# Kernel optimization log

Hardware: AMD Instinct MI355X
Metric: run time of the kernel (lower is better)

## Reference

```python
import jax, jax.numpy as jnp
import numpy as np

LORA_ALPHA = 16.0
TOP_K = 2


def setup_inputs() -> dict:
    key = jax.random.key(0)
    k_x, k_w, k_g, k_a, k_b = jax.random.split(key, 5)
    B, S, H, O, E, R = 2, 2048, 2048, 2048, 8, 16
    x = jax.random.normal(k_x, (B, S, H), dtype=jnp.float32)
    weight = jax.random.normal(k_w, (O, H), dtype=jnp.float32)          # frozen base W [out, in]
    gate_w = jax.random.normal(k_g, (E, H), dtype=jnp.float32) * 0.02   # router gate [E, in]
    A_w = jax.random.normal(k_a, (E, R, H), dtype=jnp.float32) * (1.0 / np.sqrt(H))  # stacked lora_A
    B_w = jax.random.normal(k_b, (E, O, R), dtype=jnp.float32) * 0.01   # stacked lora_B
    return {"x": x, "weight": weight, "gate_w": gate_w, "A_w": A_w, "B_w": B_w}


def reference(x, weight, gate_w, A_w, B_w):
    E = gate_w.shape[0]
    # Base frozen linear: F.linear(x, weight)
    out = jnp.einsum("bsh,oh->bso", x, weight)

    # Router: softmax over experts, top-2, renormalize
    logits = jnp.einsum("bsh,eh->bse", x, gate_w)
    probs = jax.nn.softmax(logits, axis=-1)
    topk_w, topk_idx = jax.lax.top_k(probs, TOP_K)          # [b,s,2]
    topk_w = topk_w / jnp.sum(topk_w, axis=-1, keepdims=True)

    # Per-token combine weight for each expert (sum over the 2 slots)
    onehot = jax.nn.one_hot(topk_idx, E, dtype=x.dtype)      # [b,s,2,E]
    cw = jnp.einsum("bsk,bske->bse", topk_w, onehot)         # [b,s,E]

    # LoRA: down-project into all experts' rank spaces, weight, then up-project.
    # t: [b,s,E,r] is small (r=16); weighting here avoids a [b,s,E,out] buffer.
    t = jnp.einsum("bsh,erh->bser", x, A_w)
    t = t * cw[..., None]
    lora = jnp.einsum("bser,eor->bso", t, B_w)

    return out + LORA_ALPHA * lora
```

## Files before the change

kernel.cpp:

```cpp
#include <hip/hip_runtime.h>
#include <hip/hip_bf16.h>


typedef __bf16 bf16x8 __attribute__((ext_vector_type(8)));
typedef float f32x4 __attribute__((ext_vector_type(4)));

__device__ __forceinline__ __bf16 f2bf(float f) {
  union { float f; unsigned u; } v; v.f = f;
  unsigned r = (v.u + 0x7FFFu + ((v.u >> 16) & 1u)) >> 16;
  unsigned short s = (unsigned short)r;
  return __builtin_bit_cast(__bf16, s);
}

__device__ __forceinline__ void ld_lds16(const void* g, void* l) {
  __builtin_amdgcn_global_load_lds((__attribute__((address_space(1))) void*)g,
                                   (__attribute__((address_space(3))) void*)l,
                                   16, 0, 0);
}

__global__ void prep_kernel(const float* __restrict__ W, const float* __restrict__ Aw,
                            const float* __restrict__ Bw, __bf16* __restrict__ Bfull,
                            __bf16* __restrict__ A2) {
  const int b = blockIdx.x, tid = threadIdx.x;
  if (b < 2176) {
    const float* src = (b < 2048) ? (W + (size_t)b * 2048)
                                  : (Aw + (size_t)(b - 2048) * 2048);
    __bf16* dst = (b < 2048) ? (Bfull + (size_t)b * 2176)
                             : (A2 + (size_t)(b - 2048) * 2048);
    const int c = tid * 8;
    float4 a = *(const float4*)(src + c);
    float4 d = *(const float4*)(src + c + 4);
    bf16x8 v;
    v[0] = f2bf(a.x); v[1] = f2bf(a.y); v[2] = f2bf(a.z); v[3] = f2bf(a.w);
    v[4] = f2bf(d.x); v[5] = f2bf(d.y); v[6] = f2bf(d.z); v[7] = f2bf(d.w);
    *(bf16x8*)(dst + c) = v;
  } else {
    const int idx = (b - 2176) * 256 + tid;
    const int e = idx >> 11, o = idx & 2047;
    const float4* s = (const float4*)(Bw + ((size_t)e * 2048 + o) * 16);
    float4 v0 = s[0], v1 = s[1], v2 = s[2], v3 = s[3];
    __bf16* d = Bfull + (size_t)o * 2176 + 2048 + e * 16;
    bf16x8 lo, hi;
    lo[0] = f2bf(v0.x); lo[1] = f2bf(v0.y); lo[2] = f2bf(v0.z); lo[3] = f2bf(v0.w);
    lo[4] = f2bf(v1.x); lo[5] = f2bf(v1.y); lo[6] = f2bf(v1.z); lo[7] = f2bf(v1.w);
    hi[0] = f2bf(v2.x); hi[1] = f2bf(v2.y); hi[2] = f2bf(v2.z); hi[3] = f2bf(v2.w);
    hi[4] = f2bf(v3.x); hi[5] = f2bf(v3.y); hi[6] = f2bf(v3.z); hi[7] = f2bf(v3.w);
    *(bf16x8*)d = lo;
    *(bf16x8*)(d + 8) = hi;
  }
}

__global__ __launch_bounds__(256) void router_t2(
    const float* __restrict__ x, const float* __restrict__ gw,
    const __bf16* __restrict__ A2, __bf16* __restrict__ Abuf) {
  __shared__ __align__(16) __bf16 xs[16][2056];
  __shared__ float red[4][16][8];
  __shared__ float cws[16][8];
  const int tid = threadIdx.x;
  const int wave = tid >> 6, lane = tid & 63;
  const int t0 = blockIdx.x * 16;

#pragma unroll 4
  for (int i = 0; i < 16; ++i) {
    const float* xr = x + (size_t)(t0 + i) * 2048 + tid * 8;
    float4 a = *(const float4*)xr;
    float4 b = *(const float4*)(xr + 4);
    bf16x8 v;
    v[0] = f2bf(a.x); v[1] = f2bf(a.y); v[2] = f2bf(a.z); v[3] = f2bf(a.w);
    v[4] = f2bf(b.x); v[5] = f2bf(b.y); v[6] = f2bf(b.z); v[7] = f2bf(b.w);
    *(bf16x8*)(Abuf + (size_t)(t0 + i) * 2176 + tid * 8) = v;
    *(bf16x8*)&xs[i][tid * 8] = v;
  }
  __syncthreads();

  const int tok = tid & 15, slc = tid >> 4;
  const int c0 = slc * 128;
  float acc[8] = {0, 0, 0, 0, 0, 0, 0, 0};
  for (int j8 = 0; j8 < 16; ++j8) {
    bf16x8 xv = *(const bf16x8*)&xs[tok][c0 + j8 * 8];
    float xf[8];
#pragma unroll
    for (int j = 0; j < 8; ++j) xf[j] = (float)xv[j];
#pragma unroll
    for (int e = 0; e < 8; ++e) {
      float4 g0 = *(const float4*)(gw + e * 2048 + c0 + j8 * 8);
      float4 g1 = *(const float4*)(gw + e * 2048 + c0 + j8 * 8 + 4);
      acc[e] += xf[0] * g0.x + xf[1] * g0.y + xf[2] * g0.z + xf[3] * g0.w +
                xf[4] * g1.x + xf[5] * g1.y + xf[6] * g1.z + xf[7] * g1.w;
    }
  }
#pragma unroll
  for (int e = 0; e < 8; ++e) {
    acc[e] += __shfl_down(acc[e], 16);
    acc[e] += __shfl_down(acc[e], 32);
  }
  if (lane < 16) {
#pragma unroll
    for (int e = 0; e < 8; ++e) red[wave][lane][e] = acc[e];
  }
  __syncthreads();
  if (tid < 16) {
    float lg[8];
#pragma unroll
    for (int e = 0; e < 8; ++e)
      lg[e] = red[0][tid][e] + red[1][tid][e] + red[2][tid][e] + red[3][tid][e];
    int a = 0;
    for (int e = 1; e < 8; ++e) if (lg[e] > lg[a]) a = e;
    int b = (a == 0) ? 1 : 0;
    for (int e = 0; e < 8; ++e) if (e != a && lg[e] > lg[b]) b = e;
    const float d = __expf(lg[b] - lg[a]);
    float o[8] = {0, 0, 0, 0, 0, 0, 0, 0};
    o[a] = 1.0f / (1.0f + d);
    o[b] = d / (1.0f + d);
#pragma unroll
    for (int e = 0; e < 8; ++e) cws[tid][e] = o[e];
  }
  __syncthreads();

  const int m = lane & 15, q = lane >> 4;
  const int nt0 = wave * 2;
  f32x4 tacc[2] = {};
  for (int ks = 0; ks < 64; ++ks) {
    bf16x8 af = *(const bf16x8*)&xs[m][ks * 32 + q * 8];
#pragma unroll
    for (int h = 0; h < 2; ++h) {
      bf16x8 bfg = *(const bf16x8*)(A2 + (size_t)((nt0 + h) * 16 + m) * 2048 +
                                    ks * 32 + q * 8);
      tacc[h] = __builtin_amdgcn_mfma_f32_16x16x32_bf16(af, bfg, tacc[h], 0, 0, 0);
    }
  }
#pragma unroll
  for (int h = 0; h < 2; ++h) {
    const int nt = nt0 + h;
#pragma unroll
    for (int rg = 0; rg < 4; ++rg) {
      const int trow = q * 4 + rg;
      const float s = tacc[h][rg] * 16.0f * cws[trow][nt];
      Abuf[(size_t)(t0 + trow) * 2176 + 2048 + nt * 16 + m] = f2bf(s);
    }
  }
}

__global__ __launch_bounds__(128, 2) void mfma_gemm_bt(
    const __bf16* __restrict__ A, const __bf16* __restrict__ B,
    float* __restrict__ C, int lda, int ldb, int ldc, int kiters) {
  __shared__ __align__(16) __bf16 As[128 * 64];
  __shared__ __align__(16) __bf16 Bs[64 * 64];
  const int tid = threadIdx.x;
  const int wave = tid >> 6;
  const int lane = tid & 63;
  const int tm = blockIdx.x * 128;
  const int tn = blockIdx.y * 64;

  const int wm = wave * 64;
  const int srow = lane >> 3;
  const int skoff = ((lane & 7) ^ srow) * 8;

  const int rlo = lane & 7;
  const int rb3 = (lane >> 3) & 1;
  const int qb = lane >> 4;

  f32x4 acc[4][4] = {};

  int kcur = 0;
  for (int kt = 0; kt < kiters; ++kt) {
#pragma unroll
    for (int r = 0; r < 8; ++r) {
      const int ch = r * 2 + wave;
      ld_lds16(A + (size_t)(tm + ch * 8 + srow) * lda + kcur + skoff, &As[ch * 512]);
    }
#pragma unroll
    for (int r = 0; r < 4; ++r) {
      const int ch = r * 2 + wave;
      ld_lds16(B + (size_t)(tn + ch * 8 + srow) * ldb + kcur + skoff, &Bs[ch * 512]);
    }
    __syncthreads();
#pragma unroll
    for (int ks = 0; ks < 2; ++ks) {
      bf16x8 af[4], bfg[4];
      const int q8 = ((ks * 4 + qb) ^ rlo) * 8;
#pragma unroll
      for (int i = 0; i < 4; ++i) {
        const int rh = ((wm + i * 16) >> 3) + rb3;
        af[i] = *(const bf16x8*)&As[rh * 512 + rlo * 64 + q8];
      }
#pragma unroll
      for (int j = 0; j < 4; ++j) {
        const int rh = ((j * 16) >> 3) + rb3;
        bfg[j] = *(const bf16x8*)&Bs[rh * 512 + rlo * 64 + q8];
      }
#pragma unroll
      for (int i = 0; i < 4; ++i)
#pragma unroll
        for (int j = 0; j < 4; ++j)
          acc[i][j] = __builtin_amdgcn_mfma_f32_16x16x32_bf16(af[i], bfg[j], acc[i][j], 0, 0, 0);
    }
    __syncthreads();
    kcur += 64;
  }

  const int crow0 = tm + wm + (lane >> 4) * 4;
  const int ccol0 = tn + (lane & 15);
#pragma unroll
  for (int i = 0; i < 4; ++i)
#pragma unroll
    for (int j = 0; j < 4; ++j)
#pragma unroll
      for (int rg = 0; rg < 4; ++rg)
        C[(size_t)(crow0 + i * 16 + rg) * ldc + ccol0 + j * 16] = acc[i][j][rg];
}

extern "C" void kernel_launch(void* const* d_in, const int* in_sizes, int n_in,
                              void* d_out, int out_size, void* d_ws, size_t ws_size,
                              hipStream_t stream) {
  const float* x = (const float*)d_in[0];
  const float* weight = (const float*)d_in[1];
  const float* gate_w = (const float*)d_in[2];
  const float* A_w = (const float*)d_in[3];
  const float* B_w = (const float*)d_in[4];
  float* out = (float*)d_out;

  char* ws = (char*)d_ws;
  __bf16* Abuf = (__bf16*)ws;
  __bf16* Bfull = (__bf16*)(ws + 17825792);
  __bf16* A2 = (__bf16*)(ws + 26738688);

  prep_kernel<<<2240, 256, 0, stream>>>(weight, A_w, B_w, Bfull, A2);
  router_t2<<<256, 256, 0, stream>>>(x, gate_w, A2, Abuf);
  mfma_gemm_bt<<<dim3(32, 32), 128, 0, stream>>>(Abuf, Bfull, out, 2176, 2176,
                                                 2048, 34);
}
```

Before: 166.5 us.

## Split router into convert/route and LoRA-down kernels; use four waves in GEMM

```diff
diff --git a/kernel.cpp b/kernel.cpp
--- a/kernel.cpp
+++ b/kernel.cpp
@@ -50,60 +50,62 @@
   }
 }
 
-__global__ __launch_bounds__(256) void router_t2(
+__global__ __launch_bounds__(256) void conv_router(
     const float* __restrict__ x, const float* __restrict__ gw,
-    const __bf16* __restrict__ A2, __bf16* __restrict__ Abuf) {
-  __shared__ __align__(16) __bf16 xs[16][2056];
-  __shared__ float red[4][16][8];
-  __shared__ float cws[16][8];
+    __bf16* __restrict__ Abuf, float* __restrict__ cw) {
+  __shared__ float red[256][17];
+  __shared__ float red2[16][17];
   const int tid = threadIdx.x;
-  const int wave = tid >> 6, lane = tid & 63;
-  const int t0 = blockIdx.x * 16;
-
-#pragma unroll 4
-  for (int i = 0; i < 16; ++i) {
-    const float* xr = x + (size_t)(t0 + i) * 2048 + tid * 8;
-    float4 a = *(const float4*)xr;
-    float4 b = *(const float4*)(xr + 4);
-    bf16x8 v;
-    v[0] = f2bf(a.x); v[1] = f2bf(a.y); v[2] = f2bf(a.z); v[3] = f2bf(a.w);
-    v[4] = f2bf(b.x); v[5] = f2bf(b.y); v[6] = f2bf(b.z); v[7] = f2bf(b.w);
-    *(bf16x8*)(Abuf + (size_t)(t0 + i) * 2176 + tid * 8) = v;
-    *(bf16x8*)&xs[i][tid * 8] = v;
-  }
+  const int t0 = blockIdx.x * 2;
+  const int c = tid * 8;
+
+  float4 a0 = *(const float4*)(x + (size_t)t0 * 2048 + c);
+  float4 b0 = *(const float4*)(x + (size_t)t0 * 2048 + c + 4);
+  float4 a1 = *(const float4*)(x + (size_t)(t0 + 1) * 2048 + c);
+  float4 b1 = *(const float4*)(x + (size_t)(t0 + 1) * 2048 + c + 4);
+  float xf0[8] = {a0.x, a0.y, a0.z, a0.w, b0.x, b0.y, b0.z, b0.w};
+  float xf1[8] = {a1.x, a1.y, a1.z, a1.w, b1.x, b1.y, b1.z, b1.w};
+
+  bf16x8 v0, v1;
+#pragma unroll
+  for (int j = 0; j < 8; ++j) { v0[j] = f2bf(xf0[j]); v1[j] = f2bf(xf1[j]); }
+  *(bf16x8*)(Abuf + (size_t)t0 * 2176 + c) = v0;
+  *(bf16x8*)(Abuf + (size_t)(t0 + 1) * 2176 + c) = v1;
+
+  float acc0[8], acc1[8];
+#pragma unroll
+  for (int e = 0; e < 8; ++e) { acc0[e] = 0.0f; acc1[e] = 0.0f; }
+#pragma unroll
+  for (int e = 0; e < 8; ++e) {
+    float4 g0 = *(const float4*)(gw + e * 2048 + c);
+    float4 g1 = *(const float4*)(gw + e * 2048 + c + 4);
+    float gg[8] = {g0.x, g0.y, g0.z, g0.w, g1.x, g1.y, g1.z, g1.w};
+#pragma unroll
+    for (int j = 0; j < 8; ++j) {
+      acc0[e] += xf0[j] * gg[j];
+      acc1[e] += xf1[j] * gg[j];
+    }
+  }
+#pragma unroll
+  for (int e = 0; e < 8; ++e) { red[tid][e] = acc0[e]; red[tid][8 + e] = acc1[e]; }
   __syncthreads();
-
-  const int tok = tid & 15, slc = tid >> 4;
-  const int c0 = slc * 128;
-  float acc[8] = {0, 0, 0, 0, 0, 0, 0, 0};
-  for (int j8 = 0; j8 < 16; ++j8) {
-    bf16x8 xv = *(const bf16x8*)&xs[tok][c0 + j8 * 8];
-    float xf[8];
-#pragma unroll
-    for (int j = 0; j < 8; ++j) xf[j] = (float)xv[j];
+  {
+    const int p = tid & 15, ch = tid >> 4;
+    float s = 0.0f;
+#pragma unroll
+    for (int i = 0; i < 16; ++i) s += red[ch * 16 + i][p];
+    red2[ch][p] = s;
+  }
+  __syncthreads();
+  if (tid < 2) {
+    float lg[8];
 #pragma unroll
     for (int e = 0; e < 8; ++e) {
-      float4 g0 = *(const float4*)(gw + e * 2048 + c0 + j8 * 8);
-      float4 g1 = *(const float4*)(gw + e * 2048 + c0 + j8 * 8 + 4);
-      acc[e] += xf[0] * g0.x + xf[1] * g0.y + xf[2] * g0.z + xf[3] * g0.w +
-                xf[4] * g1.x + xf[5] * g1.y + xf[6] * g1.z + xf[7] * g1.w;
-    }
-  }
-#pragma unroll
-  for (int e = 0; e < 8; ++e) {
-    acc[e] += __shfl_down(acc[e], 16);
-    acc[e] += __shfl_down(acc[e], 32);
-  }
-  if (lane < 16) {
-#pragma unroll
-    for (int e = 0; e < 8; ++e) red[wave][lane][e] = acc[e];
-  }
-  __syncthreads();
-  if (tid < 16) {
-    float lg[8];
-#pragma unroll
-    for (int e = 0; e < 8; ++e)
-      lg[e] = red[0][tid][e] + red[1][tid][e] + red[2][tid][e] + red[3][tid][e];
+      float s = 0.0f;
+#pragma unroll
+      for (int ch = 0; ch < 16; ++ch) s += red2[ch][tid * 8 + e];
+      lg[e] = s;
+    }
     int a = 0;
     for (int e = 1; e < 8; ++e) if (lg[e] > lg[a]) a = e;
     int b = (a == 0) ? 1 : 0;
@@ -112,36 +114,41 @@
     float o[8] = {0, 0, 0, 0, 0, 0, 0, 0};
     o[a] = 1.0f / (1.0f + d);
     o[b] = d / (1.0f + d);
-#pragma unroll
-    for (int e = 0; e < 8; ++e) cws[tid][e] = o[e];
-  }
-  __syncthreads();
-
+    const int t = t0 + tid;
+#pragma unroll
+    for (int e = 0; e < 8; ++e) cw[t * 8 + e] = o[e];
+  }
+}
+
+__global__ __launch_bounds__(256) void t2_scale(
+    const __bf16* __restrict__ Abuf_x, const __bf16* __restrict__ A2,
+    const float* __restrict__ cw, __bf16* __restrict__ Abuf) {
+  const int tid = threadIdx.x;
+  const int wave = tid >> 6, lane = tid & 63;
+  const int t0 = blockIdx.x * 16;
+  const int jg = blockIdx.y * 4 + wave;
   const int m = lane & 15, q = lane >> 4;
-  const int nt0 = wave * 2;
-  f32x4 tacc[2] = {};
-  for (int ks = 0; ks < 64; ++ks) {
-    bf16x8 af = *(const bf16x8*)&xs[m][ks * 32 + q * 8];
-#pragma unroll
-    for (int h = 0; h < 2; ++h) {
-      bf16x8 bfg = *(const bf16x8*)(A2 + (size_t)((nt0 + h) * 16 + m) * 2048 +
-                                    ks * 32 + q * 8);
-      tacc[h] = __builtin_amdgcn_mfma_f32_16x16x32_bf16(af, bfg, tacc[h], 0, 0, 0);
-    }
-  }
-#pragma unroll
-  for (int h = 0; h < 2; ++h) {
-    const int nt = nt0 + h;
-#pragma unroll
-    for (int rg = 0; rg < 4; ++rg) {
-      const int trow = q * 4 + rg;
-      const float s = tacc[h][rg] * 16.0f * cws[trow][nt];
-      Abuf[(size_t)(t0 + trow) * 2176 + 2048 + nt * 16 + m] = f2bf(s);
-    }
-  }
-}
-
-__global__ __launch_bounds__(128, 2) void mfma_gemm_bt(
+
+  const __bf16* arow = Abuf_x + (size_t)(t0 + m) * 2176 + q * 8;
+  const __bf16* brow = A2 + (size_t)(jg * 16 + m) * 2048 + q * 8;
+  f32x4 acc0 = {}, acc1 = {};
+  for (int ks = 0; ks < 64; ks += 2) {
+    bf16x8 af0 = *(const bf16x8*)(arow + ks * 32);
+    bf16x8 bf0 = *(const bf16x8*)(brow + ks * 32);
+    bf16x8 af1 = *(const bf16x8*)(arow + ks * 32 + 32);
+    bf16x8 bf1 = *(const bf16x8*)(brow + ks * 32 + 32);
+    acc0 = __builtin_amdgcn_mfma_f32_16x16x32_bf16(af0, bf0, acc0, 0, 0, 0);
+    acc1 = __builtin_amdgcn_mfma_f32_16x16x32_bf16(af1, bf1, acc1, 0, 0, 0);
+  }
+#pragma unroll
+  for (int rg = 0; rg < 4; ++rg) {
+    const int t = t0 + q * 4 + rg;
+    const float s = (acc0[rg] + acc1[rg]) * 16.0f * cw[t * 8 + jg];
+    Abuf[(size_t)t * 2176 + 2048 + jg * 16 + m] = f2bf(s);
+  }
+}
+
+__global__ __launch_bounds__(256, 4) void mfma_gemm_bt(
     const __bf16* __restrict__ A, const __bf16* __restrict__ B,
     float* __restrict__ C, int lda, int ldb, int ldc, int kiters) {
   __shared__ __align__(16) __bf16 As[128 * 64];
@@ -152,7 +159,8 @@
   const int tm = blockIdx.x * 128;
   const int tn = blockIdx.y * 64;
 
-  const int wm = wave * 64;
+  const int wm = (wave >> 1) * 64;
+  const int wn = (wave & 1) * 32;
   const int srow = lane >> 3;
   const int skoff = ((lane & 7) ^ srow) * 8;
 
@@ -160,24 +168,24 @@
   const int rb3 = (lane >> 3) & 1;
   const int qb = lane >> 4;
 
-  f32x4 acc[4][4] = {};
+  f32x4 acc[4][2] = {};
 
   int kcur = 0;
   for (int kt = 0; kt < kiters; ++kt) {
 #pragma unroll
-    for (int r = 0; r < 8; ++r) {
-      const int ch = r * 2 + wave;
+    for (int r = 0; r < 4; ++r) {
+      const int ch = r * 4 + wave;
       ld_lds16(A + (size_t)(tm + ch * 8 + srow) * lda + kcur + skoff, &As[ch * 512]);
     }
 #pragma unroll
-    for (int r = 0; r < 4; ++r) {
-      const int ch = r * 2 + wave;
+    for (int r = 0; r < 2; ++r) {
+      const int ch = r * 4 + wave;
       ld_lds16(B + (size_t)(tn + ch * 8 + srow) * ldb + kcur + skoff, &Bs[ch * 512]);
     }
     __syncthreads();
 #pragma unroll
     for (int ks = 0; ks < 2; ++ks) {
-      bf16x8 af[4], bfg[4];
+      bf16x8 af[4], bfg[2];
       const int q8 = ((ks * 4 + qb) ^ rlo) * 8;
 #pragma unroll
       for (int i = 0; i < 4; ++i) {
@@ -185,14 +193,14 @@
         af[i] = *(const bf16x8*)&As[rh * 512 + rlo * 64 + q8];
       }
 #pragma unroll
-      for (int j = 0; j < 4; ++j) {
-        const int rh = ((j * 16) >> 3) + rb3;
+      for (int j = 0; j < 2; ++j) {
+        const int rh = ((wn + j * 16) >> 3) + rb3;
         bfg[j] = *(const bf16x8*)&Bs[rh * 512 + rlo * 64 + q8];
       }
 #pragma unroll
       for (int i = 0; i < 4; ++i)
 #pragma unroll
-        for (int j = 0; j < 4; ++j)
+        for (int j = 0; j < 2; ++j)
           acc[i][j] = __builtin_amdgcn_mfma_f32_16x16x32_bf16(af[i], bfg[j], acc[i][j], 0, 0, 0);
     }
     __syncthreads();
@@ -200,11 +208,11 @@
   }
 
   const int crow0 = tm + wm + (lane >> 4) * 4;
-  const int ccol0 = tn + (lane & 15);
+  const int ccol0 = tn + wn + (lane & 15);
 #pragma unroll
   for (int i = 0; i < 4; ++i)
 #pragma unroll
-    for (int j = 0; j < 4; ++j)
+    for (int j = 0; j < 2; ++j)
 #pragma unroll
       for (int rg = 0; rg < 4; ++rg)
         C[(size_t)(crow0 + i * 16 + rg) * ldc + ccol0 + j * 16] = acc[i][j][rg];
@@ -224,9 +232,11 @@
   __bf16* Abuf = (__bf16*)ws;
   __bf16* Bfull = (__bf16*)(ws + 17825792);
   __bf16* A2 = (__bf16*)(ws + 26738688);
+  float* cw = (float*)(ws + 27262976);
 
   prep_kernel<<<2240, 256, 0, stream>>>(weight, A_w, B_w, Bfull, A2);
-  router_t2<<<256, 256, 0, stream>>>(x, gate_w, A2, Abuf);
-  mfma_gemm_bt<<<dim3(32, 32), 128, 0, stream>>>(Abuf, Bfull, out, 2176, 2176,
+  conv_router<<<2048, 256, 0, stream>>>(x, gate_w, Abuf, cw);
+  t2_scale<<<dim3(256, 2), 256, 0, stream>>>(Abuf, A2, cw, Abuf);
+  mfma_gemm_bt<<<dim3(32, 32), 256, 0, stream>>>(Abuf, Bfull, out, 2176, 2176,
                                                  2048, 34);
 }
```

Result: slower. 181.6 us (+9.1%).
